# Performance work log

Hardware: AMD Instinct MI355X
Metric: run time of the kernel (lower is better)

The kernel has to match this reference:

```python
import jax, jax.numpy as jnp
import numpy as np

N = 100000      # nodes
E = 1600000     # random edges (self-loops appended, as PyG GATConv does)
IN = 128        # in_channels
HID = 8         # hidden_channels per head
HEADS = 8
OUT = 40        # out_channels (classes)
NEG_SLOPE = 0.2 # PyG GATConv default


def _xavier(k, shape, fan_in, fan_out):
    lim = np.sqrt(6.0 / (fan_in + fan_out)).astype(np.float32)
    return jax.random.uniform(k, shape, jnp.float32, -lim, lim)


def setup_inputs() -> dict:
    key = jax.random.key(0)
    ks = jax.random.split(key, 8)
    x = jax.random.normal(ks[0], (N, IN), jnp.float32)
    ei = jax.random.randint(ks[1], (2, E), 0, N)
    loops = jnp.arange(N)
    edge_index = jnp.concatenate([ei, jnp.stack([loops, loops])], axis=1)  # [2, E+N]
    W1 = _xavier(ks[2], (HEADS * HID, IN), IN, HEADS * HID)
    att_src1 = _xavier(ks[3], (HEADS, HID), HID, 1)
    att_dst1 = _xavier(ks[4], (HEADS, HID), HID, 1)
    b1 = jnp.zeros((HEADS * HID,), jnp.float32)
    W2 = _xavier(ks[5], (OUT, HEADS * HID), HEADS * HID, OUT)
    att_src2 = _xavier(ks[6], (1, OUT), OUT, 1)
    att_dst2 = _xavier(ks[7], (1, OUT), OUT, 1)
    b2 = jnp.zeros((OUT,), jnp.float32)
    return {"x": x, "edge_index": edge_index, "W1": W1, "att_src1": att_src1,
            "att_dst1": att_dst1, "b1": b1, "W2": W2, "att_src2": att_src2,
            "att_dst2": att_dst2, "b2": b2}


def _gat_conv(x, src, dst, W, a_src, a_dst, b, heads, ch, concat):
    n = x.shape[0]
    h = (x @ W.T).reshape(n, heads, ch)                       # [N,H,C]
    a_s = jnp.sum(h * a_src[None], axis=-1)                   # [N,H]
    a_d = jnp.sum(h * a_dst[None], axis=-1)                   # [N,H]
    e = jax.nn.leaky_relu(a_s[src] + a_d[dst], NEG_SLOPE)     # [Eall,H]
    # segment softmax over edges sharing a destination node
    e_max = jax.ops.segment_max(e, dst, num_segments=n)
    ex = jnp.exp(e - e_max[dst])
    denom = jax.ops.segment_sum(ex, dst, num_segments=n)
    alpha = ex / denom[dst]                                   # [Eall,H]
    msg = h[src] * alpha[:, :, None]                          # [Eall,H,C]
    out = jax.ops.segment_sum(msg, dst, num_segments=n)       # [N,H,C]
    out = out.reshape(n, heads * ch) if concat else out.mean(axis=1)
    return out + b


def reference(x, edge_index, W1, att_src1, att_dst1, b1, W2, att_src2, att_dst2, b2):
    # eval mode: dropout is identity
    src, dst = edge_index[0], edge_index[1]
    h = _gat_conv(x, src, dst, W1, att_src1, att_dst1, b1, HEADS, HID, True)
    h = jax.nn.elu(h)
    out = _gat_conv(h, src, dst, W2, att_src2, att_dst2, b2, 1, OUT, False)
    return out
```

## Files before the change

### kernel.cpp

```cpp
#include <hip/hip_runtime.h>
#include <hip/hip_bf16.h>

#define IN_CH   128
#define HID     8
#define HEADS   8
#define C1      64
#define OUT_CH  40
#define NEG     0.2f
#define NPART   8

typedef __attribute__((ext_vector_type(8))) short  short8;
typedef __attribute__((ext_vector_type(4))) float  f32x4;

__device__ __forceinline__ float b2f(unsigned short u) {
    return __uint_as_float(((unsigned int)u) << 16);
}
__device__ __forceinline__ float blo(unsigned int p) { return __uint_as_float(p << 16); }
__device__ __forceinline__ float bhi(unsigned int p) { return __uint_as_float(p & 0xffff0000u); }
__device__ __forceinline__ unsigned short f2b(float f) {
    unsigned int u = __float_as_uint(f);
    unsigned int r = (u + 0x7fffu + ((u >> 16) & 1u)) >> 16;
    return (unsigned short)r;
}
__device__ __forceinline__ float lrelu(float v) { return v > 0.f ? v : NEG * v; }

#define P_W1    0
#define P_AS1   8192
#define P_AD1   8256
#define P_B1    8320
#define P_W2    8384
#define P_AS2   10944
#define P_AD2   10984
#define P_B2    11024
#define P_TOT   11064

__global__ __launch_bounds__(256) void k0_detect(
        const unsigned int* __restrict__ x32,
        const void* W1, const void* as1, const void* ad1, const void* b1,
        const void* W2, const void* as2, const void* ad2, const void* b2,
        int* __restrict__ flag, float* __restrict__ pf,
        unsigned short* __restrict__ w1bf) {
    int t = threadIdx.x;
    __shared__ int sflag;
    if (t < 64) {
        unsigned int lo = x32[t] & 0xffffu;
        int ex = (int)((lo >> 7) & 0xff);
        bool sane = (ex >= 112 && ex <= 143);
        unsigned long long m = __ballot(sane);
        if (t == 0) {
            int isbf = (__popcll(m) >= 32) ? 1 : 0;
            sflag = isbf;
            *flag = isbf;
        }
    }
    __syncthreads();
    const int isbf = sflag;
#define CONV(dstoff, srcp, cnt)                                         \
    if (isbf) {                                                         \
        const unsigned short* sp = (const unsigned short*)(srcp);       \
        for (int i = t; i < (cnt); i += 256) pf[(dstoff) + i] = b2f(sp[i]); \
    } else {                                                            \
        const float* sp = (const float*)(srcp);                         \
        for (int i = t; i < (cnt); i += 256) pf[(dstoff) + i] = sp[i];  \
    }
    CONV(P_W1,  W1, 8192)
    CONV(P_AS1, as1, 64)
    CONV(P_AD1, ad1, 64)
    CONV(P_B1,  b1, 64)
    CONV(P_W2,  W2, 2560)
    CONV(P_AS2, as2, 40)
    CONV(P_AD2, ad2, 40)
    CONV(P_B2,  b2, 40)
#undef CONV
    if (isbf) {
        const unsigned short* sp = (const unsigned short*)W1;
        for (int i = t; i < 8192; i += 256) w1bf[i] = sp[i];
    } else {
        const float* sp = (const float*)W1;
        for (int i = t; i < 8192; i += 256) w1bf[i] = f2b(sp[i]);
    }
}

__global__ __launch_bounds__(256) void kA_hist(
        const int* __restrict__ dst, int* __restrict__ deg,
        int e_all, int n_nodes) {
    int part = blockIdx.x & (NPART - 1);
    int nm   = gridDim.x >> 3;
    int mblk = blockIdx.x >> 3;
    int lo = (int)((long long)part * n_nodes / NPART);
    int hi = (int)((long long)(part + 1) * n_nodes / NPART);
    for (int e = mblk * 256 + threadIdx.x; e < e_all; e += nm * 256) {
        int d = dst[e];
        if (d >= lo && d < hi) atomicAdd(&deg[d], 1);
    }
}

__global__ __launch_bounds__(256) void kB1_scan(
        const int* __restrict__ deg, int* __restrict__ offs,
        int* __restrict__ bsum, int n) {
    __shared__ int sd[256];
    int t = threadIdx.x;
    int i = blockIdx.x * 256 + t;
    int v = (i < n) ? deg[i] : 0;
    sd[t] = v;
    __syncthreads();
    for (int off = 1; off < 256; off <<= 1) {
        int u = (t >= off) ? sd[t - off] : 0;
        __syncthreads();
        sd[t] += u;
        __syncthreads();
    }
    if (i < n) offs[i] = sd[t] - v;
    if (t == 255) bsum[blockIdx.x] = sd[255];
}

__global__ __launch_bounds__(512) void kB2_scanb(
        const int* __restrict__ bsum, int* __restrict__ bsumx, int nb) {
    __shared__ int sd[512];
    int t = threadIdx.x;
    int v = (t < nb) ? bsum[t] : 0;
    sd[t] = v;
    __syncthreads();
    for (int off = 1; off < 512; off <<= 1) {
        int u = (t >= off) ? sd[t - off] : 0;
        __syncthreads();
        sd[t] += u;
        __syncthreads();
    }
    if (t < nb) bsumx[t] = sd[t] - v;
}

__global__ __launch_bounds__(256) void kB3_fix(
        int* __restrict__ offs, const int* __restrict__ bsumx,
        int* __restrict__ cursor, int n) {
    int i = blockIdx.x * 256 + threadIdx.x;
    if (i >= n) return;
    int o = offs[i] + bsumx[blockIdx.x];
    offs[i] = o;
    cursor[i] = o;
}

__global__ __launch_bounds__(256) void kC_scatter(
        const int* __restrict__ src, const int* __restrict__ dst,
        int* __restrict__ cursor, int* __restrict__ csr_src,
        int e_all, int n_nodes) {
    int part = blockIdx.x & (NPART - 1);
    int nm   = gridDim.x >> 3;
    int mblk = blockIdx.x >> 3;
    int lo = (int)((long long)part * n_nodes / NPART);
    int hi = (int)((long long)(part + 1) * n_nodes / NPART);
    for (int e = mblk * 256 + threadIdx.x; e < e_all; e += nm * 256) {
        int d = dst[e];
        if (d >= lo && d < hi) {
            int pos = atomicAdd(&cursor[d], 1);
            csr_src[pos] = src[e];
        }
    }
}

__global__ __launch_bounds__(256) void k1_mfma(
        const void* __restrict__ x, const unsigned short* __restrict__ w1bf,
        const float* __restrict__ pf, const int* __restrict__ flagp,
        unsigned short* __restrict__ h1b, float* __restrict__ as1, float* __restrict__ ad1,
        int n_nodes) {
    int tid = threadIdx.x;
    int wv = tid >> 6, L = tid & 63;
    int m = L & 15, q = L >> 4;
    int base = blockIdx.x * 64 + wv * 16;
    if (base >= n_nodes) return;
    const int isbf = *flagp;

    short8 bfr[4][4];
#pragma unroll
    for (int t = 0; t < 4; ++t)
#pragma unroll
        for (int kb = 0; kb < 4; ++kb)
            bfr[t][kb] = *(const short8*)(w1bf + (size_t)(t * 16 + m) * IN_CH + kb * 32 + q * 8);

    int row = base + m;
    if (row >= n_nodes) row = n_nodes - 1;
    short8 af[4];
    if (isbf) {
        const unsigned short* xr = (const unsigned short*)x + (size_t)row * IN_CH + q * 8;
#pragma unroll
        for (int kb = 0; kb < 4; ++kb) af[kb] = *(const short8*)(xr + kb * 32);
    } else {
        const float* xr = (const float*)x + (size_t)row * IN_CH + q * 8;
#pragma unroll
        for (int kb = 0; kb < 4; ++kb) {
            short8 a;
#pragma unroll
            for (int j = 0; j < 8; ++j) a[j] = (short)f2b(xr[kb * 32 + j]);
            af[kb] = a;
        }
    }

    f32x4 acc[4];
#pragma unroll
    for (int t = 0; t < 4; ++t) acc[t] = (f32x4){0.f, 0.f, 0.f, 0.f};
#pragma unroll
    for (int t = 0; t < 4; ++t)
#pragma unroll
        for (int kb = 0; kb < 4; ++kb)
            acc[t] = __builtin_amdgcn_mfma_f32_16x16x32_bf16(af[kb], bfr[t][kb], acc[t], 0, 0, 0);

#pragma unroll
    for (int t = 0; t < 4; ++t) {
#pragma unroll
        for (int r = 0; r < 4; ++r) {
            int node = base + q * 4 + r;
            bool ok = (node < n_nodes);
            float val = acc[t][r];
            int ch = t * 16 + m;
            if (ok) h1b[(size_t)node * C1 + ch] = f2b(val);
            float ps = val * pf[P_AS1 + ch];
            float pd = val * pf[P_AD1 + ch];
            ps += __shfl_xor(ps, 1, 64); ps += __shfl_xor(ps, 2, 64); ps += __shfl_xor(ps, 4, 64);
            pd += __shfl_xor(pd, 1, 64); pd += __shfl_xor(pd, 2, 64); pd += __shfl_xor(pd, 4, 64);
            if (ok && (L & 7) == 0) {
                int head = 2 * t + ((m >> 3) & 1);
                as1[(size_t)node * HEADS + head] = ps;
                ad1[(size_t)node * HEADS + head] = pd;
            }
        }
    }
}

__global__ __launch_bounds__(256) void k3_fused1(
        const int* __restrict__ offs, const int* __restrict__ deg,
        const int* __restrict__ csr_src,
        const float* __restrict__ as1, const float* __restrict__ ad1,
        const unsigned short* __restrict__ h1b, const float* __restrict__ pf,
        unsigned short* __restrict__ x2, int n_nodes) {
    int d = blockIdx.x * 4 + (threadIdx.x >> 6);
    if (d >= n_nodes) return;
    int t = threadIdx.x & 63;
    int head = t >> 3;
    int j8 = t >> 3, h8 = t & 7;
    float adv1 = ad1[(size_t)d * HEADS + h8];
    int start = offs[d];
    int dg = deg[d];
    float acc = 0.f, den = 0.f;
    int nfull = dg & ~7;
    int base = 0;
    for (; base < nfull; base += 8) {
        int s = csr_src[start + base + j8];
        float v = as1[(size_t)s * HEADS + h8] + adv1;
        float w = __expf(lrelu(v));
#pragma unroll
        for (int jj = 0; jj < 8; ++jj) {
            int sj   = __shfl(s, jj * 8, 64);
            float wj = __shfl(w, jj * 8 + head, 64);
            float hv = b2f(h1b[(size_t)sj * C1 + t]);
            den += wj;
            acc += wj * hv;
        }
    }
    int rem = dg - nfull;
    if (rem) {
        int s = 0; float w = 0.f;
        if (j8 < rem) {
            s = csr_src[start + base + j8];
            float v = as1[(size_t)s * HEADS + h8] + adv1;
            w = __expf(lrelu(v));
        }
        for (int jj = 0; jj < rem; ++jj) {
            int sj   = __shfl(s, jj * 8, 64);
            float wj = __shfl(w, jj * 8 + head, 64);
            float hv = b2f(h1b[(size_t)sj * C1 + t]);
            den += wj;
            acc += wj * hv;
        }
    }
    float o = acc / den + pf[P_B1 + t];
    o = o > 0.f ? o : (__expf(o) - 1.f);
    x2[(size_t)d * C1 + t] = f2b(o);
}

__global__ __launch_bounds__(256) void k4_gemm2(
        const unsigned short* __restrict__ x2, const float* __restrict__ pf,
        unsigned short* __restrict__ h2b, float* __restrict__ as2, float* __restrict__ ad2,
        int n_nodes) {
    int tid = threadIdx.x;
    int w = tid >> 6, t = tid & 63;
    __shared__ float wTf[4096];
    __shared__ float xsf[4 * C1];
    for (int e = tid; e < 2560; e += 256) {
        int row = e >> 6, k = e & 63;
        int g = k >> 2, j = k & 3;
        wTf[(g * 64 + ((row + g) & 63)) * 4 + j] = pf[P_W2 + e];
    }
    __syncthreads();
    const float4* wT4 = (const float4*)wTf;
    int base = blockIdx.x * 32 + w * 8;
    for (int i = 0; i < 8; ++i) {
        int n = base + i;
        bool ok = (n < n_nodes);
        if (ok && t < 32) {
            unsigned int p = ((const unsigned int*)x2)[(size_t)n * 32 + t];
            xsf[w * C1 + 2 * t]     = blo(p);
            xsf[w * C1 + 2 * t + 1] = bhi(p);
        }
        __syncthreads();
        if (ok) {
            float hs = 0.f, hd = 0.f;
            if (t < OUT_CH) {
                const float4* xv = (const float4*)(xsf + w * C1);
                float acc = 0.f;
#pragma unroll
                for (int g = 0; g < 16; ++g) {
                    float4 wv = wT4[g * 64 + ((t + g) & 63)];
                    float4 x4 = xv[g];
                    acc += x4.x * wv.x + x4.y * wv.y + x4.z * wv.z + x4.w * wv.w;
                }
                h2b[(size_t)n * OUT_CH + t] = f2b(acc);
                hs = acc * pf[P_AS2 + t];
                hd = acc * pf[P_AD2 + t];
            }
            for (int off = 1; off < 64; off <<= 1) {
                hs += __shfl_xor(hs, off, 64);
                hd += __shfl_xor(hd, off, 64);
            }
            if (t == 0) { as2[n] = hs; ad2[n] = hd; }
        }
        __syncthreads();
    }
}

__global__ __launch_bounds__(256) void k6_fused2(
        const int* __restrict__ offs, const int* __restrict__ deg,
        const int* __restrict__ csr_src,
        const float* __restrict__ as2, const float* __restrict__ ad2,
        const unsigned short* __restrict__ h2b, const float* __restrict__ pf,
        const int* __restrict__ flagp, void* __restrict__ outp, int n_nodes) {
    int d = blockIdx.x * 4 + (threadIdx.x >> 6);
    if (d >= n_nodes) return;
    int t = threadIdx.x & 63;
    float adv = ad2[d];
    int start = offs[d];
    int dg = deg[d];
    bool act = (t < OUT_CH);
    int tc = act ? t : 0;
    float acc = 0.f, den = 0.f;
    int nfull = dg & ~15;
    int base = 0;
    for (; base < nfull; base += 16) {
        int s = 0; float w = 0.f;
        if (t < 16) {
            s = csr_src[start + base + t];
            w = __expf(lrelu(as2[s] + adv));
        }
#pragma unroll
        for (int jj = 0; jj < 16; ++jj) {
            int sj   = __shfl(s, jj, 64);
            float wj = __shfl(w, jj, 64);
            float hv = b2f(h2b[(size_t)sj * OUT_CH + tc]);
            den += wj;
            acc += wj * hv;
        }
    }
    int rem = dg - nfull;
    if (rem) {
        int s = 0; float w = 0.f;
        if (t < rem) {
            s = csr_src[start + base + t];
            w = __expf(lrelu(as2[s] + adv));
        }
        for (int jj = 0; jj < rem; ++jj) {
            int sj   = __shfl(s, jj, 64);
            float wj = __shfl(w, jj, 64);
            float hv = b2f(h2b[(size_t)sj * OUT_CH + tc]);
            den += wj;
            acc += wj * hv;
        }
    }
    if (!act) return;
    float o = acc / den + pf[P_B2 + t];
    size_t idx = (size_t)d * OUT_CH + t;
    if (*flagp) ((unsigned short*)outp)[idx] = f2b(o);
    else        ((float*)outp)[idx] = o;
}

extern "C" void kernel_launch(void* const* d_in, const int* in_sizes, int n_in,
                              void* d_out, int out_size, void* d_ws, size_t ws_size,
                              hipStream_t stream) {
    const void* x  = d_in[0];
    const int*  ei = (const int*)d_in[1];

    const int n_nodes = in_sizes[0] / IN_CH;
    const int e_all   = in_sizes[1] / 2;
    const int* srcI = ei;
    const int* dstI = ei + e_all;

    float* ws = (float*)d_ws;
    const size_t n = (size_t)n_nodes;
    int* deg     = (int*)ws;
    int* offs    = deg + n;
    int* cursor  = offs + n;
    int* bsum    = cursor + n;
    int* bsumx   = bsum + 512;
    int* csr_src = bsumx + 512;
    float* A     = ws + 3 * n + 1024 + (size_t)e_all;
    float* as1   = A;
    float* ad1   = A + 8 * n;
    unsigned short* h1b = (unsigned short*)(A + 16 * n);
    unsigned short* x2  = (unsigned short*)(A + 48 * n);
    int*   flagp = (int*)(A + 80 * n);
    float* pf    = A + 80 * n + 16;
    unsigned short* w1bf = (unsigned short*)(pf + P_TOT);
    float* as2 = as1;
    float* ad2 = ad1;
    unsigned short* h2b = h1b;

    k0_detect<<<1, 256, 0, stream>>>((const unsigned int*)x,
        d_in[2], d_in[3], d_in[4], d_in[5], d_in[6], d_in[7], d_in[8], d_in[9],
        flagp, pf, w1bf);

    hipMemsetAsync(deg, 0, n * sizeof(int), stream);

    kA_hist<<<1024, 256, 0, stream>>>(dstI, deg, e_all, n_nodes);

    int nb = (n_nodes + 255) / 256;
    kB1_scan<<<nb, 256, 0, stream>>>(deg, offs, bsum, n_nodes);
    kB2_scanb<<<1, 512, 0, stream>>>(bsum, bsumx, nb);
    kB3_fix<<<nb, 256, 0, stream>>>(offs, bsumx, cursor, n_nodes);

    kC_scatter<<<1024, 256, 0, stream>>>(srcI, dstI, cursor, csr_src, e_all, n_nodes);

    k1_mfma<<<(n_nodes + 63) / 64, 256, 0, stream>>>(x, w1bf, pf, flagp, h1b, as1, ad1, n_nodes);

    k3_fused1<<<(n_nodes + 3) / 4, 256, 0, stream>>>(offs, deg, csr_src, as1, ad1, h1b, pf, x2, n_nodes);

    int gb = (n_nodes + 31) / 32;
    k4_gemm2<<<gb, 256, 0, stream>>>(x2, pf, h2b, as2, ad2, n_nodes);

    k6_fused2<<<(n_nodes + 3) / 4, 256, 0, stream>>>(offs, deg, csr_src, as2, ad2, h2b, pf, flagp, d_out, n_nodes);
}
```

Baseline: 475.1 us.

## Fuse layer-1 aggregation with layer-2 GEMM and merge param prep into histogram

Merges the layer-1 aggregation kernel with the layer-2 linear projection, so the ELU output goes straight through shared memory into the 64x40 matmul. This removes the x2 intermediate round trip through global memory and one launch. The parameter-conversion kernel is folded into the degree-histogram kernel, and both the histogram and the scatter now read dst as int4. The cost is that each 4-node block restages the whole W2 transpose into LDS (about 16KB), which repeats across 25k blocks and may lower occupancy.

Result: no change. 466.0 us (-1.9%).

```diff
diff --git a/kernel.cpp b/kernel.cpp
--- a/kernel.cpp
+++ b/kernel.cpp
@@ -34,12 +34,14 @@
 #define P_B2    11024
 #define P_TOT   11064
 
-__global__ __launch_bounds__(256) void k0_detect(
+__global__ __launch_bounds__(256) void kA_fused(
         const unsigned int* __restrict__ x32,
-        const void* W1, const void* as1, const void* ad1, const void* b1,
-        const void* W2, const void* as2, const void* ad2, const void* b2,
+        const void* W1, const void* as1p, const void* ad1p, const void* b1,
+        const void* W2, const void* as2p, const void* ad2p, const void* b2,
+        const int* __restrict__ dst, int* __restrict__ deg,
         int* __restrict__ flag, float* __restrict__ pf,
-        unsigned short* __restrict__ w1bf) {
+        unsigned short* __restrict__ w1bf,
+        int e_all, int n_nodes) {
     int t = threadIdx.x;
     __shared__ int sflag;
     if (t < 64) {
@@ -50,46 +52,55 @@
         if (t == 0) {
             int isbf = (__popcll(m) >= 32) ? 1 : 0;
             sflag = isbf;
-            *flag = isbf;
+            if (blockIdx.x == 0) *flag = isbf;
         }
     }
     __syncthreads();
     const int isbf = sflag;
+
+    if (blockIdx.x < 8) {
+        int g = blockIdx.x * 256 + t;
 #define CONV(dstoff, srcp, cnt)                                         \
-    if (isbf) {                                                         \
-        const unsigned short* sp = (const unsigned short*)(srcp);       \
-        for (int i = t; i < (cnt); i += 256) pf[(dstoff) + i] = b2f(sp[i]); \
-    } else {                                                            \
-        const float* sp = (const float*)(srcp);                         \
-        for (int i = t; i < (cnt); i += 256) pf[(dstoff) + i] = sp[i];  \
-    }
-    CONV(P_W1,  W1, 8192)
-    CONV(P_AS1, as1, 64)
-    CONV(P_AD1, ad1, 64)
-    CONV(P_B1,  b1, 64)
-    CONV(P_W2,  W2, 2560)
-    CONV(P_AS2, as2, 40)
-    CONV(P_AD2, ad2, 40)
-    CONV(P_B2,  b2, 40)
+        if (isbf) {                                                     \
+            const unsigned short* sp = (const unsigned short*)(srcp);   \
+            for (int i = g; i < (cnt); i += 2048) pf[(dstoff) + i] = b2f(sp[i]); \
+        } else {                                                        \
+            const float* sp = (const float*)(srcp);                     \
+            for (int i = g; i < (cnt); i += 2048) pf[(dstoff) + i] = sp[i]; \
+        }
+        CONV(P_W1,  W1, 8192)
+        CONV(P_AS1, as1p, 64)
+        CONV(P_AD1, ad1p, 64)
+        CONV(P_B1,  b1, 64)
+        CONV(P_W2,  W2, 2560)
+        CONV(P_AS2, as2p, 40)
+        CONV(P_AD2, ad2p, 40)
+        CONV(P_B2,  b2, 40)
 #undef CONV
-    if (isbf) {
-        const unsigned short* sp = (const unsigned short*)W1;
-        for (int i = t; i < 8192; i += 256) w1bf[i] = sp[i];
-    } else {
-        const float* sp = (const float*)W1;
-        for (int i = t; i < 8192; i += 256) w1bf[i] = f2b(sp[i]);
-    }
-}
-
-__global__ __launch_bounds__(256) void kA_hist(
-        const int* __restrict__ dst, int* __restrict__ deg,
-        int e_all, int n_nodes) {
+        if (isbf) {
+            const unsigned short* sp = (const unsigned short*)W1;
+            for (int i = g; i < 8192; i += 2048) w1bf[i] = sp[i];
+        } else {
+            const float* sp = (const float*)W1;
+            for (int i = g; i < 8192; i += 2048) w1bf[i] = f2b(sp[i]);
+        }
+    }
+
     int part = blockIdx.x & (NPART - 1);
     int nm   = gridDim.x >> 3;
     int mblk = blockIdx.x >> 3;
     int lo = (int)((long long)part * n_nodes / NPART);
     int hi = (int)((long long)(part + 1) * n_nodes / NPART);
-    for (int e = mblk * 256 + threadIdx.x; e < e_all; e += nm * 256) {
+    const int4* dst4 = (const int4*)dst;
+    int e4n = e_all >> 2;
+    for (int i = mblk * 256 + t; i < e4n; i += nm * 256) {
+        int4 d4 = dst4[i];
+        if (d4.x >= lo && d4.x < hi) atomicAdd(&deg[d4.x], 1);
+        if (d4.y >= lo && d4.y < hi) atomicAdd(&deg[d4.y], 1);
+        if (d4.z >= lo && d4.z < hi) atomicAdd(&deg[d4.z], 1);
+        if (d4.w >= lo && d4.w < hi) atomicAdd(&deg[d4.w], 1);
+    }
+    for (int e = (e4n << 2) + mblk * 256 + t; e < e_all; e += nm * 256) {
         int d = dst[e];
         if (d >= lo && d < hi) atomicAdd(&deg[d], 1);
     }
@@ -149,12 +160,19 @@
     int mblk = blockIdx.x >> 3;
     int lo = (int)((long long)part * n_nodes / NPART);
     int hi = (int)((long long)(part + 1) * n_nodes / NPART);
-    for (int e = mblk * 256 + threadIdx.x; e < e_all; e += nm * 256) {
+    const int4* dst4 = (const int4*)dst;
+    int e4n = e_all >> 2;
+    for (int i = mblk * 256 + threadIdx.x; i < e4n; i += nm * 256) {
+        int4 d4 = dst4[i];
+        int eb = i << 2;
+        if (d4.x >= lo && d4.x < hi) { int p = atomicAdd(&cursor[d4.x], 1); csr_src[p] = src[eb]; }
+        if (d4.y >= lo && d4.y < hi) { int p = atomicAdd(&cursor[d4.y], 1); csr_src[p] = src[eb + 1]; }
+        if (d4.z >= lo && d4.z < hi) { int p = atomicAdd(&cursor[d4.z], 1); csr_src[p] = src[eb + 2]; }
+        if (d4.w >= lo && d4.w < hi) { int p = atomicAdd(&cursor[d4.w], 1); csr_src[p] = src[eb + 3]; }
+    }
+    for (int e = (e4n << 2) + mblk * 256 + threadIdx.x; e < e_all; e += nm * 256) {
         int d = dst[e];
-        if (d >= lo && d < hi) {
-            int pos = atomicAdd(&cursor[d], 1);
-            csr_src[pos] = src[e];
-        }
+        if (d >= lo && d < hi) { int p = atomicAdd(&cursor[d], 1); csr_src[p] = src[e]; }
     }
 }
 
@@ -226,15 +244,26 @@
     }
 }
 
-__global__ __launch_bounds__(256) void k3_fused1(
+__global__ __launch_bounds__(256) void k34_fused(
         const int* __restrict__ offs, const int* __restrict__ deg,
         const int* __restrict__ csr_src,
         const float* __restrict__ as1, const float* __restrict__ ad1,
         const unsigned short* __restrict__ h1b, const float* __restrict__ pf,
-        unsigned short* __restrict__ x2, int n_nodes) {
-    int d = blockIdx.x * 4 + (threadIdx.x >> 6);
+        unsigned short* __restrict__ h2b, float* __restrict__ as2v, float* __restrict__ ad2v,
+        int n_nodes) {
+    int tid = threadIdx.x;
+    int w = tid >> 6, t = tid & 63;
+    __shared__ float wTf[4096];
+    __shared__ float xsf[4 * C1];
+    for (int e = tid; e < 2560; e += 256) {
+        int row = e >> 6, k = e & 63;
+        int g = k >> 2, j = k & 3;
+        wTf[(g * 64 + ((row + g) & 63)) * 4 + j] = pf[P_W2 + e];
+    }
+    __syncthreads();
+    int d = blockIdx.x * 4 + w;
     if (d >= n_nodes) return;
-    int t = threadIdx.x & 63;
+
     int head = t >> 3;
     int j8 = t >> 3, h8 = t & 7;
     float adv1 = ad1[(size_t)d * HEADS + h8];
@@ -246,11 +275,11 @@
     for (; base < nfull; base += 8) {
         int s = csr_src[start + base + j8];
         float v = as1[(size_t)s * HEADS + h8] + adv1;
-        float w = __expf(lrelu(v));
+        float wgt = __expf(lrelu(v));
 #pragma unroll
         for (int jj = 0; jj < 8; ++jj) {
             int sj   = __shfl(s, jj * 8, 64);
-            float wj = __shfl(w, jj * 8 + head, 64);
+            float wj = __shfl(wgt, jj * 8 + head, 64);
             float hv = b2f(h1b[(size_t)sj * C1 + t]);
             den += wj;
             acc += wj * hv;
@@ -258,15 +287,15 @@
     }
     int rem = dg - nfull;
     if (rem) {
-        int s = 0; float w = 0.f;
+        int s = 0; float wgt = 0.f;
         if (j8 < rem) {
             s = csr_src[start + base + j8];
             float v = as1[(size_t)s * HEADS + h8] + adv1;
-            w = __expf(lrelu(v));
+            wgt = __expf(lrelu(v));
         }
         for (int jj = 0; jj < rem; ++jj) {
             int sj   = __shfl(s, jj * 8, 64);
-            float wj = __shfl(w, jj * 8 + head, 64);
+            float wj = __shfl(wgt, jj * 8 + head, 64);
             float hv = b2f(h1b[(size_t)sj * C1 + t]);
             den += wj;
             acc += wj * hv;
@@ -274,57 +303,28 @@
     }
     float o = acc / den + pf[P_B1 + t];
     o = o > 0.f ? o : (__expf(o) - 1.f);
-    x2[(size_t)d * C1 + t] = f2b(o);
-}
-
-__global__ __launch_bounds__(256) void k4_gemm2(
-        const unsigned short* __restrict__ x2, const float* __restrict__ pf,
-        unsigned short* __restrict__ h2b, float* __restrict__ as2, float* __restrict__ ad2,
-        int n_nodes) {
-    int tid = threadIdx.x;
-    int w = tid >> 6, t = tid & 63;
-    __shared__ float wTf[4096];
-    __shared__ float xsf[4 * C1];
-    for (int e = tid; e < 2560; e += 256) {
-        int row = e >> 6, k = e & 63;
-        int g = k >> 2, j = k & 3;
-        wTf[(g * 64 + ((row + g) & 63)) * 4 + j] = pf[P_W2 + e];
-    }
-    __syncthreads();
+    xsf[w * C1 + t] = o;
+
     const float4* wT4 = (const float4*)wTf;
-    int base = blockIdx.x * 32 + w * 8;
-    for (int i = 0; i < 8; ++i) {
-        int n = base + i;
-        bool ok = (n < n_nodes);
-        if (ok && t < 32) {
-            unsigned int p = ((const unsigned int*)x2)[(size_t)n * 32 + t];
-            xsf[w * C1 + 2 * t]     = blo(p);
-            xsf[w * C1 + 2 * t + 1] = bhi(p);
-        }
-        __syncthreads();
-        if (ok) {
-            float hs = 0.f, hd = 0.f;
-            if (t < OUT_CH) {
-                const float4* xv = (const float4*)(xsf + w * C1);
-                float acc = 0.f;
-#pragma unroll
-                for (int g = 0; g < 16; ++g) {
-                    float4 wv = wT4[g * 64 + ((t + g) & 63)];
-                    float4 x4 = xv[g];
-                    acc += x4.x * wv.x + x4.y * wv.y + x4.z * wv.z + x4.w * wv.w;
-                }
-                h2b[(size_t)n * OUT_CH + t] = f2b(acc);
-                hs = acc * pf[P_AS2 + t];
-                hd = acc * pf[P_AD2 + t];
-            }
-            for (int off = 1; off < 64; off <<= 1) {
-                hs += __shfl_xor(hs, off, 64);
-                hd += __shfl_xor(hd, off, 64);
-            }
-            if (t == 0) { as2[n] = hs; ad2[n] = hd; }
-        }
-        __syncthreads();
-    }
+    float hs = 0.f, hd = 0.f;
+    if (t < OUT_CH) {
+        const float4* xv = (const float4*)(xsf + w * C1);
+        float a2 = 0.f;
+#pragma unroll
+        for (int g = 0; g < 16; ++g) {
+            float4 wv = wT4[g * 64 + ((t + g) & 63)];
+            float4 x4 = xv[g];
+            a2 += x4.x * wv.x + x4.y * wv.y + x4.z * wv.z + x4.w * wv.w;
+        }
+        h2b[(size_t)d * OUT_CH + t] = f2b(a2);
+        hs = a2 * pf[P_AS2 + t];
+        hd = a2 * pf[P_AD2 + t];
+    }
+    for (int off = 1; off < 64; off <<= 1) {
+        hs += __shfl_xor(hs, off, 64);
+        hd += __shfl_xor(hd, off, 64);
+    }
+    if (t == 0) { as2v[d] = hs; ad2v[d] = hd; }
 }
 
 __global__ __launch_bounds__(256) void k6_fused2(
@@ -404,21 +404,18 @@
     float* as1   = A;
     float* ad1   = A + 8 * n;
     unsigned short* h1b = (unsigned short*)(A + 16 * n);
-    unsigned short* x2  = (unsigned short*)(A + 48 * n);
-    int*   flagp = (int*)(A + 80 * n);
-    float* pf    = A + 80 * n + 16;
+    float* as2   = A + 48 * n;
+    float* ad2   = A + 49 * n;
+    unsigned short* h2b = (unsigned short*)(A + 50 * n);
+    int*   flagp = (int*)(A + 70 * n);
+    float* pf    = A + 70 * n + 16;
     unsigned short* w1bf = (unsigned short*)(pf + P_TOT);
-    float* as2 = as1;
-    float* ad2 = ad1;
-    unsigned short* h2b = h1b;
-
-    k0_detect<<<1, 256, 0, stream>>>((const unsigned int*)x,
+
+    hipMemsetAsync(deg, 0, n * sizeof(int), stream);
+
+    kA_fused<<<1024, 256, 0, stream>>>((const unsigned int*)x,
         d_in[2], d_in[3], d_in[4], d_in[5], d_in[6], d_in[7], d_in[8], d_in[9],
-        flagp, pf, w1bf);
-
-    hipMemsetAsync(deg, 0, n * sizeof(int), stream);
-
-    kA_hist<<<1024, 256, 0, stream>>>(dstI, deg, e_all, n_nodes);
+        dstI, deg, flagp, pf, w1bf, e_all, n_nodes);
 
     int nb = (n_nodes + 255) / 256;
     kB1_scan<<<nb, 256, 0, stream>>>(deg, offs, bsum, n_nodes);
@@ -429,10 +426,7 @@
 
     k1_mfma<<<(n_nodes + 63) / 64, 256, 0, stream>>>(x, w1bf, pf, flagp, h1b, as1, ad1, n_nodes);
 
-    k3_fused1<<<(n_nodes + 3) / 4, 256, 0, stream>>>(offs, deg, csr_src, as1, ad1, h1b, pf, x2, n_nodes);
-
-    int gb = (n_nodes + 31) / 32;
-    k4_gemm2<<<gb, 256, 0, stream>>>(x2, pf, h2b, as2, ad2, n_nodes);
+    k34_fused<<<(n_nodes + 3) / 4, 256, 0, stream>>>(offs, deg, csr_src, as1, ad1, h1b, pf, h2b, as2, ad2, n_nodes);
 
     k6_fused2<<<(n_nodes + 3) / 4, 256, 0, stream>>>(offs, deg, csr_src, as2, ad2, h2b, pf, flagp, d_out, n_nodes);
 }
```
